# Kernel tuning notes

Measured on AMD Instinct MI355X. Metric: run time of the kernel, lower is better.

The kernel has to match this reference:

```python
import jax, jax.numpy as jnp
import numpy as np

N_NODES = 50000
IN_CH = 128
HIDDEN = 64
HEADS = 2
OUT_CH = 40
N_EDGES = 800000
NEG_SLOPE = 0.2


def gat_layer(x, src, dst, W, att_src, att_dst, bias, concat):
    # x: [N, F_in]; src/dst: [E] (self-loops already appended)
    N = x.shape[0]
    H, C = att_src.shape
    h = (x @ W).reshape(N, H, C)                      # [N, H, C]
    a_s = (h * att_src[None]).sum(-1)                 # [N, H]
    a_d = (h * att_dst[None]).sum(-1)                 # [N, H]
    e = jax.nn.leaky_relu(a_s[src] + a_d[dst], NEG_SLOPE)   # [E, H]
    # numerically-stable segment softmax over incoming edges per dst node
    m = jax.ops.segment_max(e, dst, num_segments=N)   # [N, H]
    m = jnp.where(jnp.isfinite(m), m, 0.0)
    m = jax.lax.stop_gradient(m)
    ex = jnp.exp(e - m[dst])                          # [E, H]
    denom = jax.ops.segment_sum(ex, dst, num_segments=N)    # [N, H]
    alpha = ex / (denom[dst] + 1e-16)                 # [E, H]
    out = jax.ops.segment_sum(alpha[:, :, None] * h[src], dst, num_segments=N)  # [N, H, C]
    out = out.reshape(N, H * C) if concat else out.mean(axis=1)
    return out + bias


def setup_inputs() -> dict:
    key = jax.random.key(0)
    ks = jax.random.split(key, 10)
    node_feat = jax.random.normal(ks[0], (N_NODES, IN_CH), dtype=jnp.float32)
    edge_index = jax.random.randint(ks[1], (2, N_EDGES), 0, N_NODES, dtype=jnp.int64)
    s1 = 1.0 / np.sqrt(IN_CH)
    s2 = 1.0 / np.sqrt(HIDDEN * HEADS)
    return {
        "node_feat": node_feat,
        "edge_index": edge_index,
        "W1": jax.random.normal(ks[2], (IN_CH, HEADS * HIDDEN), dtype=jnp.float32) * s1,
        "att_src1": jax.random.normal(ks[3], (HEADS, HIDDEN), dtype=jnp.float32) * s1,
        "att_dst1": jax.random.normal(ks[4], (HEADS, HIDDEN), dtype=jnp.float32) * s1,
        "b1": jnp.zeros((HEADS * HIDDEN,), dtype=jnp.float32),
        "W2": jax.random.normal(ks[5], (HEADS * HIDDEN, OUT_CH), dtype=jnp.float32) * s2,
        "att_src2": jax.random.normal(ks[6], (1, OUT_CH), dtype=jnp.float32) * s2,
        "att_dst2": jax.random.normal(ks[7], (1, OUT_CH), dtype=jnp.float32) * s2,
        "b2": jnp.zeros((OUT_CH,), dtype=jnp.float32),
    }


def reference(node_feat, edge_index, W1, att_src1, att_dst1, b1, W2, att_src2, att_dst2, b2):
    N = node_feat.shape[0]
    loop = jnp.arange(N, dtype=edge_index.dtype)
    src = jnp.concatenate([edge_index[0], loop])  # add self loops (PyG default)
    dst = jnp.concatenate([edge_index[1], loop])
    # eval mode: dropout is identity; use_bn=False
    x = gat_layer(node_feat, src, dst, W1, att_src1, att_dst1, b1, concat=True)
    x = jax.nn.elu(x)
    x = gat_layer(x, src, dst, W2, att_src2, att_dst2, b2, concat=False)
    return x
```

## Files before the change

### kernel.cpp

```cpp
#include <hip/hip_runtime.h>
#include <hip/hip_bf16.h>

#define N_NODES 50000
#define E0      800000
#define E_TOT   850000

typedef short short8 __attribute__((ext_vector_type(8)));
typedef float floatx4 __attribute__((ext_vector_type(4)));

__device__ __forceinline__ float lrelu(float x) { return x > 0.f ? x : 0.2f * x; }

__device__ __forceinline__ unsigned short f2bf(float f) {
    unsigned int u = __float_as_uint(f);
    u += 0x7fffu + ((u >> 16) & 1u);
    return (unsigned short)(u >> 16);
}
__device__ __forceinline__ float lo_bf(unsigned int p) { return __uint_as_float(p << 16); }
__device__ __forceinline__ float hi_bf(unsigned int p) { return __uint_as_float(p & 0xffff0000u); }

__device__ __forceinline__ short8 pack_bf16x8(float4 a, float4 b) {
    short8 r;
    r[0] = (short)f2bf(a.x); r[1] = (short)f2bf(a.y); r[2] = (short)f2bf(a.z); r[3] = (short)f2bf(a.w);
    r[4] = (short)f2bf(b.x); r[5] = (short)f2bf(b.y); r[6] = (short)f2bf(b.z); r[7] = (short)f2bf(b.w);
    return r;
}

__device__ __forceinline__ void fma8(float2* A, float w, uint4 h) {
    A[0].x += w * lo_bf(h.x); A[0].y += w * hi_bf(h.x);
    A[1].x += w * lo_bf(h.y); A[1].y += w * hi_bf(h.y);
    A[2].x += w * lo_bf(h.z); A[2].y += w * hi_bf(h.z);
    A[3].x += w * lo_bf(h.w); A[3].y += w * hi_bf(h.w);
}

__global__ __launch_bounds__(256) void hist_w(const int* __restrict__ ei, int* __restrict__ ghist,
                                              const float* __restrict__ W1, const float* __restrict__ W2,
                                              unsigned short* __restrict__ Wt1, unsigned short* __restrict__ Wt2) {
    __shared__ int h[256];
    int b = blockIdx.x, t = threadIdx.x;
    h[t] = 0;
    int i = b * 256 + t;
    if (i < 128 * 128) {
        int nn = i >> 7, k = i & 127;
        Wt1[i] = f2bf(W1[k * 128 + nn]);
    } else if (i < 128 * 128 + 48 * 128) {
        int j = i - 128 * 128;
        int nn = j >> 7, k = j & 127;
        Wt2[j] = (nn < 40) ? f2bf(W2[k * 40 + nn]) : (unsigned short)0;
    }
    __syncthreads();
    int base = b * 3328;
    #pragma unroll
    for (int k = 0; k < 13; ++k) {
        int e = base + t + k * 256;
        if (e < E_TOT) {
            int dst = (e < E0) ? ei[E0 + e] : (e - E0);
            atomicAdd(&h[dst >> 8], 1);
        }
    }
    __syncthreads();
    ghist[t * 256 + b] = h[t];
}

__global__ __launch_bounds__(256) void scan_local(const int* __restrict__ src, int* __restrict__ dst,
                                                  int* __restrict__ bsum, int n) {
    __shared__ int wsum[4];
    int t = threadIdx.x, lane = t & 63, wid = t >> 6;
    int idx = blockIdx.x * 1024 + t * 4;
    int4 v = make_int4(0, 0, 0, 0);
    if (idx < n) v = *reinterpret_cast<const int4*>(src + idx);
    int tsum = v.x + v.y + v.z + v.w;
    int sc = tsum;
    #pragma unroll
    for (int s = 1; s < 64; s <<= 1) {
        int up = __shfl_up(sc, s);
        if (lane >= s) sc += up;
    }
    if (lane == 63) wsum[wid] = sc;
    __syncthreads();
    int woff = 0;
    for (int w = 0; w < wid; ++w) woff += wsum[w];
    int b0 = woff + (sc - tsum);
    if (idx < n) {
        int4 o;
        o.x = b0;
        o.y = b0 + v.x;
        o.z = b0 + v.x + v.y;
        o.w = b0 + v.x + v.y + v.z;
        *reinterpret_cast<int4*>(dst + idx) = o;
    }
    if (t == 255) bsum[blockIdx.x] = woff + sc;
}

__global__ __launch_bounds__(256) void scan_addoff(int* __restrict__ arr, const int* __restrict__ bsum,
                                                   int* __restrict__ total, int n, int nb) {
    __shared__ int add_sh;
    int t = threadIdx.x;
    if (t < 64) {
        int v = (t < nb) ? bsum[t] : 0;
        int sc = v;
        #pragma unroll
        for (int s = 1; s < 64; s <<= 1) {
            int up = __shfl_up(sc, s);
            if (t >= s) sc += up;
        }
        if (t == (int)blockIdx.x) add_sh = sc - v;
        if (blockIdx.x == 0 && t == nb - 1) total[0] = sc;
    }
    __syncthreads();
    int idx = blockIdx.x * 1024 + t * 4;
    if (idx < n) {
        int add = add_sh;
        int4 v4 = *reinterpret_cast<int4*>(arr + idx);
        v4.x += add; v4.y += add; v4.z += add; v4.w += add;
        *reinterpret_cast<int4*>(arr + idx) = v4;
    }
}

__global__ __launch_bounds__(256) void scatter1(const int* __restrict__ ei, const int* __restrict__ gbase,
                                                unsigned int* __restrict__ tmpk) {
    __shared__ int cur[256];
    int b = blockIdx.x, t = threadIdx.x;
    cur[t] = gbase[t * 256 + b];
    __syncthreads();
    int base = b * 3328;
    #pragma unroll
    for (int k = 0; k < 13; ++k) {
        int e = base + t + k * 256;
        if (e < E_TOT) {
            int src, dst;
            if (e < E0) { src = ei[e]; dst = ei[E0 + e]; }
            else        { src = dst = e - E0; }
            int pos = atomicAdd(&cur[dst >> 8], 1);
            tmpk[pos] = ((unsigned)dst << 16) | (unsigned)src;
        }
    }
}

__global__ __launch_bounds__(256) void sort_w(const unsigned int* __restrict__ tmpk,
                                              const int* __restrict__ gbase,
                                              const float* __restrict__ a_s, const float* __restrict__ a_d,
                                              unsigned int* __restrict__ keys, uint4* __restrict__ ew,
                                              int* __restrict__ offs) {
    __shared__ unsigned int skey[8192];
    __shared__ unsigned int sorted[8192];
    __shared__ int h2[256], binb[256], cur2[256];
    int q = blockIdx.x, t = threadIdx.x;
    int start = gbase[q * 256];
    int end   = gbase[(q + 1) * 256];
    int n = end - start;
    if (n > 8192) n = 8192;
    h2[t] = 0;
    __syncthreads();
    for (int i = t; i < n; i += 256) {
        unsigned int k = tmpk[start + i];
        skey[i] = k;
        atomicAdd(&h2[(k >> 16) & 255], 1);
    }
    __syncthreads();
    if (t < 64) {
        int carry = 0;
        #pragma unroll
        for (int ch = 0; ch < 4; ++ch) {
            int idx = ch * 64 + t;
            int v = h2[idx];
            int sc = v;
            #pragma unroll
            for (int s = 1; s < 64; s <<= 1) {
                int up = __shfl_up(sc, s);
                if (t >= s) sc += up;
            }
            binb[idx] = sc - v + carry;
            cur2[idx] = sc - v + carry;
            carry += __shfl(sc, 63);
        }
    }
    __syncthreads();
    for (int i = t; i < n; i += 256) {
        unsigned int k = skey[i];
        int pos = atomicAdd(&cur2[(k >> 16) & 255], 1);
        sorted[pos] = k;
    }
    __syncthreads();
    for (int i = t; i < n; i += 256) {
        unsigned int k = sorted[i];
        keys[start + i] = k;
        int src = k & 0xFFFF, dst = k >> 16;
        float2 av = *reinterpret_cast<const float2*>(&a_s[src * 2]);
        float2 dv = *reinterpret_cast<const float2*>(&a_d[dst * 2]);
        uint4 e;
        e.x = k;
        e.y = __float_as_uint(__expf(lrelu(av.x + dv.x)));
        e.z = __float_as_uint(__expf(lrelu(av.y + dv.y)));
        e.w = 0;
        ew[start + i] = e;
    }
    int idx = q * 256 + t;
    if (idx <= N_NODES) offs[idx] = start + binb[t];
}

__global__ __launch_bounds__(256) void gemm1_mfma(const float* __restrict__ X, const unsigned short* __restrict__ Wt,
                                                  const float* __restrict__ asw, const float* __restrict__ adw,
                                                  unsigned short* __restrict__ h1b, float* __restrict__ a_s,
                                                  float* __restrict__ a_d, int nRows) {
    int t = threadIdx.x, lane = t & 63, wave = t >> 6;
    int l15 = lane & 15, g = lane >> 4;
    int r0 = blockIdx.x * 64;
    int row = r0 + wave * 16 + l15;
    bool rv = row < nRows;
    const float* xrow = X + (size_t)(rv ? row : 0) * 128;

    float asv[8], adv[8];
    #pragma unroll
    for (int nt = 0; nt < 8; ++nt) { asv[nt] = asw[nt * 16 + l15]; adv[nt] = adw[nt * 16 + l15]; }

    floatx4 acc[8];
    #pragma unroll
    for (int nt = 0; nt < 8; ++nt) acc[nt] = (floatx4){0.f, 0.f, 0.f, 0.f};

    #pragma unroll
    for (int ks = 0; ks < 4; ++ks) {
        float4 xa = *reinterpret_cast<const float4*>(xrow + ks * 32 + g * 8);
        float4 xb = *reinterpret_cast<const float4*>(xrow + ks * 32 + g * 8 + 4);
        short8 af = pack_bf16x8(xa, xb);
        #pragma unroll
        for (int nt = 0; nt < 8; ++nt) {
            short8 bf = *reinterpret_cast<const short8*>(Wt + (size_t)(nt * 16 + l15) * 128 + ks * 32 + g * 8);
            acc[nt] = __builtin_amdgcn_mfma_f32_16x16x32_bf16(af, bf, acc[nt], 0, 0, 0);
        }
    }

    #pragma unroll
    for (int i = 0; i < 4; ++i) {
        int gr = r0 + wave * 16 + g * 4 + i;
        float s0 = 0.f, d0 = 0.f, s1 = 0.f, d1 = 0.f;
        #pragma unroll
        for (int nt = 0; nt < 4; ++nt) { s0 += acc[nt][i] * asv[nt]; d0 += acc[nt][i] * adv[nt]; }
        #pragma unroll
        for (int nt = 4; nt < 8; ++nt) { s1 += acc[nt][i] * asv[nt]; d1 += acc[nt][i] * adv[nt]; }
        #pragma unroll
        for (int sh = 1; sh < 16; sh <<= 1) {
            s0 += __shfl_xor(s0, sh); d0 += __shfl_xor(d0, sh);
            s1 += __shfl_xor(s1, sh); d1 += __shfl_xor(d1, sh);
        }
        if (gr < nRows) {
            if (l15 == 0) {
                a_s[gr * 2] = s0;     a_d[gr * 2] = d0;
                a_s[gr * 2 + 1] = s1; a_d[gr * 2 + 1] = d1;
            }
            #pragma unroll
            for (int nt = 0; nt < 8; ++nt)
                h1b[(size_t)gr * 128 + nt * 16 + l15] = f2bf(acc[nt][i]);
        }
    }
}

__global__ __launch_bounds__(256) void gemm2_mfma(const unsigned short* __restrict__ X2b,
                                                  const unsigned short* __restrict__ Wt,
                                                  const float* __restrict__ asw, const float* __restrict__ adw,
                                                  unsigned short* __restrict__ h2b, float* __restrict__ a_s,
                                                  float* __restrict__ a_d, int nRows) {
    int t = threadIdx.x, lane = t & 63, wave = t >> 6;
    int l15 = lane & 15, g = lane >> 4;
    int r0 = blockIdx.x * 64;
    int row = r0 + wave * 16 + l15;
    bool rv = row < nRows;
    const unsigned short* xrow = X2b + (size_t)(rv ? row : 0) * 128;

    float asv[3], adv[3];
    #pragma unroll
    for (int nt = 0; nt < 3; ++nt) {
        int col = nt * 16 + l15;
        asv[nt] = (col < 40) ? asw[col] : 0.f;
        adv[nt] = (col < 40) ? adw[col] : 0.f;
    }

    floatx4 acc[3];
    #pragma unroll
    for (int nt = 0; nt < 3; ++nt) acc[nt] = (floatx4){0.f, 0.f, 0.f, 0.f};

    #pragma unroll
    for (int ks = 0; ks < 4; ++ks) {
        short8 af = *reinterpret_cast<const short8*>(xrow + ks * 32 + g * 8);
        #pragma unroll
        for (int nt = 0; nt < 3; ++nt) {
            short8 bf = *reinterpret_cast<const short8*>(Wt + (size_t)(nt * 16 + l15) * 128 + ks * 32 + g * 8);
            acc[nt] = __builtin_amdgcn_mfma_f32_16x16x32_bf16(af, bf, acc[nt], 0, 0, 0);
        }
    }

    #pragma unroll
    for (int i = 0; i < 4; ++i) {
        int gr = r0 + wave * 16 + g * 4 + i;
        float ps = 0.f, pd = 0.f;
        #pragma unroll
        for (int nt = 0; nt < 3; ++nt) { ps += acc[nt][i] * asv[nt]; pd += acc[nt][i] * adv[nt]; }
        #pragma unroll
        for (int sh = 1; sh < 16; sh <<= 1) { ps += __shfl_xor(ps, sh); pd += __shfl_xor(pd, sh); }
        if (gr < nRows) {
            if (l15 == 0) { a_s[gr] = ps; a_d[gr] = pd; }
            #pragma unroll
            for (int nt = 0; nt < 3; ++nt) {
                int col = nt * 16 + l15;
                if (col < 40) h2b[(size_t)gr * 40 + col] = f2bf(acc[nt][i]);
            }
        }
    }
}

__global__ __launch_bounds__(256) void aggregate1(const unsigned short* __restrict__ Hb,
                                                  const uint4* __restrict__ ew, const int* __restrict__ offs,
                                                  const float* __restrict__ bias,
                                                  unsigned short* __restrict__ X2b, int n) {
    int t = threadIdx.x, lane = t & 63, wid = t >> 6;
    int node = blockIdx.x * 4 + wid;
    if (node >= n) return;
    int c = lane & 15, q = lane >> 4, head = c >> 3;
    int beg = offs[node], deg = offs[node + 1] - beg;
    float den = 0.f;
    float2 acc0[4], acc1[4];
    #pragma unroll
    for (int m = 0; m < 4; ++m) { acc0[m] = make_float2(0.f, 0.f); acc1[m] = make_float2(0.f, 0.f); }

    for (int j = 0; j < deg; j += 16) {
        int sE[4]; float wE[4];
        #pragma unroll
        for (int k2 = 0; k2 < 4; ++k2) {
            int idx = j + 4 * k2 + q;
            sE[k2] = 0; wE[k2] = 0.f;
            if (idx < deg) {
                uint4 e = ew[beg + idx];
                sE[k2] = (int)(e.x & 0xFFFF);
                wE[k2] = __uint_as_float(head ? e.z : e.y);
            }
        }
        uint4 h0 = *reinterpret_cast<const uint4*>(&Hb[(size_t)sE[0] * 128 + c * 8]);
        uint4 h1 = *reinterpret_cast<const uint4*>(&Hb[(size_t)sE[1] * 128 + c * 8]);
        uint4 h2 = *reinterpret_cast<const uint4*>(&Hb[(size_t)sE[2] * 128 + c * 8]);
        uint4 h3 = *reinterpret_cast<const uint4*>(&Hb[(size_t)sE[3] * 128 + c * 8]);
        den += wE[0] + wE[1] + wE[2] + wE[3];
        fma8(acc0, wE[0], h0);
        fma8(acc1, wE[1], h1);
        fma8(acc0, wE[2], h2);
        fma8(acc1, wE[3], h3);
    }
    #pragma unroll
    for (int m = 0; m < 4; ++m) { acc0[m].x += acc1[m].x; acc0[m].y += acc1[m].y; }
    den += __shfl_xor(den, 16); den += __shfl_xor(den, 32);
    #pragma unroll
    for (int m = 0; m < 4; ++m) {
        acc0[m].x += __shfl_xor(acc0[m].x, 16); acc0[m].x += __shfl_xor(acc0[m].x, 32);
        acc0[m].y += __shfl_xor(acc0[m].y, 16); acc0[m].y += __shfl_xor(acc0[m].y, 32);
    }
    if (q == 0) {
        float dinv = 1.f / (den + 1e-16f);
        float4 b0 = *reinterpret_cast<const float4*>(&bias[c * 8]);
        float4 b1 = *reinterpret_cast<const float4*>(&bias[c * 8 + 4]);
        float va[8] = {acc0[0].x, acc0[0].y, acc0[1].x, acc0[1].y, acc0[2].x, acc0[2].y, acc0[3].x, acc0[3].y};
        float bb[8] = {b0.x, b0.y, b0.z, b0.w, b1.x, b1.y, b1.z, b1.w};
        float o[8];
        #pragma unroll
        for (int k = 0; k < 8; ++k) {
            float v = va[k] * dinv + bb[k];
            o[k] = v > 0.f ? v : (__expf(v) - 1.f);
        }
        uint4 pk;
        pk.x = (unsigned)f2bf(o[0]) | ((unsigned)f2bf(o[1]) << 16);
        pk.y = (unsigned)f2bf(o[2]) | ((unsigned)f2bf(o[3]) << 16);
        pk.z = (unsigned)f2bf(o[4]) | ((unsigned)f2bf(o[5]) << 16);
        pk.w = (unsigned)f2bf(o[6]) | ((unsigned)f2bf(o[7]) << 16);
        *reinterpret_cast<uint4*>(&X2b[(size_t)node * 128 + c * 8]) = pk;
    }
}

__global__ __launch_bounds__(256) void aggregate2(const unsigned short* __restrict__ Hb,
                                                  const float* __restrict__ a_s, const float* __restrict__ a_d,
                                                  const int* __restrict__ offs, const unsigned int* __restrict__ keys,
                                                  const float* __restrict__ bias, float* __restrict__ out, int n) {
    int t = threadIdx.x, lane = t & 63, wid = t >> 6;
    int node = blockIdx.x * 4 + wid;
    if (node >= n) return;
    int g = lane / 5, c = lane - g * 5;
    bool dead = (g >= 12);
    if (dead) { g = 0; c = 0; }
    int beg = offs[node], deg = offs[node + 1] - beg;
    float adv = a_d[node];
    float den = 0.f;
    float2 acc0[4], acc1[4];
    #pragma unroll
    for (int m = 0; m < 4; ++m) { acc0[m] = make_float2(0.f, 0.f); acc1[m] = make_float2(0.f, 0.f); }

    for (int j = 0; j < deg; j += 24) {
        int j0 = j + g, j1 = j + 12 + g;
        int s0 = 0, s1 = 0;
        float w0 = 0.f, w1v = 0.f;
        if (!dead && j0 < deg) {
            s0 = keys[beg + j0] & 0xFFFF;
            w0 = __expf(lrelu(a_s[s0] + adv));
        }
        if (!dead && j1 < deg) {
            s1 = keys[beg + j1] & 0xFFFF;
            w1v = __expf(lrelu(a_s[s1] + adv));
        }
        uint4 h0 = *reinterpret_cast<const uint4*>(&Hb[(size_t)s0 * 40 + c * 8]);
        uint4 h1 = *reinterpret_cast<const uint4*>(&Hb[(size_t)s1 * 40 + c * 8]);
        den += w0 + w1v;
        fma8(acc0, w0, h0);
        fma8(acc1, w1v, h1);
    }
    #pragma unroll
    for (int m = 0; m < 4; ++m) { acc0[m].x += acc1[m].x; acc0[m].y += acc1[m].y; }
    den += __shfl(den, lane + 30);
    den += __shfl(den, lane + 15);
    {
        float d5 = __shfl(den, lane + 5), d10 = __shfl(den, lane + 10);
        den = den + d5 + d10;
    }
    #pragma unroll
    for (int m = 0; m < 4; ++m) {
        float ax = acc0[m].x, ay = acc0[m].y;
        ax += __shfl(ax, lane + 30); ay += __shfl(ay, lane + 30);
        ax += __shfl(ax, lane + 15); ay += __shfl(ay, lane + 15);
        float ax5 = __shfl(ax, lane + 5),  ay5 = __shfl(ay, lane + 5);
        float ax10 = __shfl(ax, lane + 10), ay10 = __shfl(ay, lane + 10);
        acc0[m].x = ax + ax5 + ax10;
        acc0[m].y = ay + ay5 + ay10;
    }
    if (lane < 5) {
        float dinv = 1.f / (den + 1e-16f);
        float4 b0 = *reinterpret_cast<const float4*>(&bias[c * 8]);
        float4 b1 = *reinterpret_cast<const float4*>(&bias[c * 8 + 4]);
        float4 o0, o1;
        o0.x = acc0[0].x * dinv + b0.x; o0.y = acc0[0].y * dinv + b0.y;
        o0.z = acc0[1].x * dinv + b0.z; o0.w = acc0[1].y * dinv + b0.w;
        o1.x = acc0[2].x * dinv + b1.x; o1.y = acc0[2].y * dinv + b1.y;
        o1.z = acc0[3].x * dinv + b1.z; o1.w = acc0[3].y * dinv + b1.w;
        *reinterpret_cast<float4*>(&out[(size_t)node * 40 + c * 8])     = o0;
        *reinterpret_cast<float4*>(&out[(size_t)node * 40 + c * 8 + 4]) = o1;
    }
}

extern "C" void kernel_launch(void* const* d_in, const int* in_sizes, int n_in,
                              void* d_out, int out_size, void* d_ws, size_t ws_size,
                              hipStream_t stream) {
    (void)in_sizes; (void)n_in; (void)out_size; (void)ws_size;
    const float* x    = (const float*)d_in[0];
    const int*   ei   = (const int*)d_in[1];
    const float* W1   = (const float*)d_in[2];
    const float* as1w = (const float*)d_in[3];
    const float* ad1w = (const float*)d_in[4];
    const float* b1   = (const float*)d_in[5];
    const float* W2   = (const float*)d_in[6];
    const float* as2w = (const float*)d_in[7];
    const float* ad2w = (const float*)d_in[8];
    const float* b2   = (const float*)d_in[9];
    float* out = (float*)d_out;

    float* ws = (float*)d_ws;
    float* h1slot = ws; ws += (size_t)N_NODES * 128;
    float* x2slot = ws; ws += (size_t)N_NODES * 128;
    float* a_s1 = ws; ws += N_NODES * 2;
    float* a_d1 = ws; ws += N_NODES * 2;
    float* a_s2 = ws; ws += N_NODES;
    float* a_d2 = ws; ws += N_NODES;
    float* h2slot = ws; ws += (size_t)N_NODES * 40;
    int* offs  = (int*)ws;
    int* ghist = offs + 50432;
    int* gbase = ghist + 65536;
    int* bsum  = gbase + 65536;
    int* total = bsum + 64;
    unsigned int* tmpk = (unsigned int*)(total + 4);
    unsigned int* keys = tmpk + E_TOT;
    uint4* ew = (uint4*)(keys + E_TOT);
    unsigned short* Wt1 = (unsigned short*)(ew + E_TOT);
    unsigned short* Wt2 = Wt1 + 128 * 128;

    unsigned short* h1b = (unsigned short*)h1slot;
    unsigned short* x2b = (unsigned short*)x2slot;
    unsigned short* h2b = (unsigned short*)h2slot;

    hist_w<<<256, 256, 0, stream>>>(ei, ghist, W1, W2, Wt1, Wt2);
    scan_local<<<64, 256, 0, stream>>>(ghist, gbase, bsum, 65536);
    scan_addoff<<<64, 256, 0, stream>>>(gbase, bsum, total, 65536, 64);
    scatter1<<<256, 256, 0, stream>>>(ei, gbase, tmpk);
    gemm1_mfma<<<(N_NODES + 63) / 64, 256, 0, stream>>>(x, Wt1, as1w, ad1w, h1b, a_s1, a_d1, N_NODES);
    sort_w<<<196, 256, 0, stream>>>(tmpk, gbase, a_s1, a_d1, keys, ew, offs);
    aggregate1<<<(N_NODES + 3) / 4, 256, 0, stream>>>(h1b, ew, offs, b1, x2b, N_NODES);
    gemm2_mfma<<<(N_NODES + 63) / 64, 256, 0, stream>>>(x2b, Wt2, as2w, ad2w, h2b, a_s2, a_d2, N_NODES);
    aggregate2<<<(N_NODES + 3) / 4, 256, 0, stream>>>(h2b, a_s2, a_d2, offs, keys, b2, out, N_NODES);
}
```

Measured before the change: 138.4 us.

## Merge gemm1 with edge scatter and stage edge metadata via wave shuffles

The separate gemm1 and scatter kernels become one launch: the first 782 blocks run the GEMM and the remaining 256 run the edge scatter, so the two independent phases share the device. In both aggregate kernels, each lane loads one edge's source index and weight (coalesced) for up to 64 or 48 edges, then broadcasts them with shuffles instead of reloading them per feature group. The softmax denominator is summed once per edge across the wave. This removes one launch boundary and redundant scattered metadata loads, at the cost of more shuffles and extra lane masking logic.

```diff
diff --git a/kernel.cpp b/kernel.cpp
--- a/kernel.cpp
+++ b/kernel.cpp
@@ -4,6 +4,7 @@
 #define N_NODES 50000
 #define E0      800000
 #define E_TOT   850000
+#define G1_BLOCKS 782
 
 typedef short short8 __attribute__((ext_vector_type(8)));
 typedef float floatx4 __attribute__((ext_vector_type(4)));
@@ -116,22 +117,86 @@
     }
 }
 
-__global__ __launch_bounds__(256) void scatter1(const int* __restrict__ ei, const int* __restrict__ gbase,
-                                                unsigned int* __restrict__ tmpk) {
+__device__ __forceinline__ void gemm1_body(int blk, const float* __restrict__ X, const unsigned short* __restrict__ Wt,
+                                           const float* __restrict__ asw, const float* __restrict__ adw,
+                                           unsigned short* __restrict__ h1b, float* __restrict__ a_s,
+                                           float* __restrict__ a_d, int nRows) {
+    int t = threadIdx.x, lane = t & 63, wave = t >> 6;
+    int l15 = lane & 15, g = lane >> 4;
+    int r0 = blk * 64;
+    int row = r0 + wave * 16 + l15;
+    bool rv = row < nRows;
+    const float* xrow = X + (size_t)(rv ? row : 0) * 128;
+
+    float asv[8], adv[8];
+    #pragma unroll
+    for (int nt = 0; nt < 8; ++nt) { asv[nt] = asw[nt * 16 + l15]; adv[nt] = adw[nt * 16 + l15]; }
+
+    floatx4 acc[8];
+    #pragma unroll
+    for (int nt = 0; nt < 8; ++nt) acc[nt] = (floatx4){0.f, 0.f, 0.f, 0.f};
+
+    #pragma unroll
+    for (int ks = 0; ks < 4; ++ks) {
+        float4 xa = *reinterpret_cast<const float4*>(xrow + ks * 32 + g * 8);
+        float4 xb = *reinterpret_cast<const float4*>(xrow + ks * 32 + g * 8 + 4);
+        short8 af = pack_bf16x8(xa, xb);
+        #pragma unroll
+        for (int nt = 0; nt < 8; ++nt) {
+            short8 bf = *reinterpret_cast<const short8*>(Wt + (size_t)(nt * 16 + l15) * 128 + ks * 32 + g * 8);
+            acc[nt] = __builtin_amdgcn_mfma_f32_16x16x32_bf16(af, bf, acc[nt], 0, 0, 0);
+        }
+    }
+
+    #pragma unroll
+    for (int i = 0; i < 4; ++i) {
+        int gr = r0 + wave * 16 + g * 4 + i;
+        float s0 = 0.f, d0 = 0.f, s1 = 0.f, d1 = 0.f;
+        #pragma unroll
+        for (int nt = 0; nt < 4; ++nt) { s0 += acc[nt][i] * asv[nt]; d0 += acc[nt][i] * adv[nt]; }
+        #pragma unroll
+        for (int nt = 4; nt < 8; ++nt) { s1 += acc[nt][i] * asv[nt]; d1 += acc[nt][i] * adv[nt]; }
+        #pragma unroll
+        for (int sh = 1; sh < 16; sh <<= 1) {
+            s0 += __shfl_xor(s0, sh); d0 += __shfl_xor(d0, sh);
+            s1 += __shfl_xor(s1, sh); d1 += __shfl_xor(d1, sh);
+        }
+        if (gr < nRows) {
+            if (l15 == 0) {
+                a_s[gr * 2] = s0;     a_d[gr * 2] = d0;
+                a_s[gr * 2 + 1] = s1; a_d[gr * 2 + 1] = d1;
+            }
+            #pragma unroll
+            for (int nt = 0; nt < 8; ++nt)
+                h1b[(size_t)gr * 128 + nt * 16 + l15] = f2bf(acc[nt][i]);
+        }
+    }
+}
+
+__global__ __launch_bounds__(256) void gemm1_scatter(const float* __restrict__ X, const unsigned short* __restrict__ Wt,
+                                                     const float* __restrict__ asw, const float* __restrict__ adw,
+                                                     unsigned short* __restrict__ h1b, float* __restrict__ a_s,
+                                                     float* __restrict__ a_d,
+                                                     const int* __restrict__ ei, const int* __restrict__ gbase,
+                                                     unsigned int* __restrict__ tmpk) {
     __shared__ int cur[256];
-    int b = blockIdx.x, t = threadIdx.x;
-    cur[t] = gbase[t * 256 + b];
-    __syncthreads();
-    int base = b * 3328;
-    #pragma unroll
-    for (int k = 0; k < 13; ++k) {
-        int e = base + t + k * 256;
-        if (e < E_TOT) {
-            int src, dst;
-            if (e < E0) { src = ei[e]; dst = ei[E0 + e]; }
-            else        { src = dst = e - E0; }
-            int pos = atomicAdd(&cur[dst >> 8], 1);
-            tmpk[pos] = ((unsigned)dst << 16) | (unsigned)src;
+    if (blockIdx.x < G1_BLOCKS) {
+        gemm1_body(blockIdx.x, X, Wt, asw, adw, h1b, a_s, a_d, N_NODES);
+    } else {
+        int b = blockIdx.x - G1_BLOCKS, t = threadIdx.x;
+        cur[t] = gbase[t * 256 + b];
+        __syncthreads();
+        int base = b * 3328;
+        #pragma unroll
+        for (int k = 0; k < 13; ++k) {
+            int e = base + t + k * 256;
+            if (e < E_TOT) {
+                int src, dst;
+                if (e < E0) { src = ei[e]; dst = ei[E0 + e]; }
+                else        { src = dst = e - E0; }
+                int pos = atomicAdd(&cur[dst >> 8], 1);
+                tmpk[pos] = ((unsigned)dst << 16) | (unsigned)src;
+            }
         }
     }
 }
@@ -198,62 +263,6 @@
     if (idx <= N_NODES) offs[idx] = start + binb[t];
 }
 
-__global__ __launch_bounds__(256) void gemm1_mfma(const float* __restrict__ X, const unsigned short* __restrict__ Wt,
-                                                  const float* __restrict__ asw, const float* __restrict__ adw,
-                                                  unsigned short* __restrict__ h1b, float* __restrict__ a_s,
-                                                  float* __restrict__ a_d, int nRows) {
-    int t = threadIdx.x, lane = t & 63, wave = t >> 6;
-    int l15 = lane & 15, g = lane >> 4;
-    int r0 = blockIdx.x * 64;
-    int row = r0 + wave * 16 + l15;
-    bool rv = row < nRows;
-    const float* xrow = X + (size_t)(rv ? row : 0) * 128;
-
-    float asv[8], adv[8];
-    #pragma unroll
-    for (int nt = 0; nt < 8; ++nt) { asv[nt] = asw[nt * 16 + l15]; adv[nt] = adw[nt * 16 + l15]; }
-
-    floatx4 acc[8];
-    #pragma unroll
-    for (int nt = 0; nt < 8; ++nt) acc[nt] = (floatx4){0.f, 0.f, 0.f, 0.f};
-
-    #pragma unroll
-    for (int ks = 0; ks < 4; ++ks) {
-        float4 xa = *reinterpret_cast<const float4*>(xrow + ks * 32 + g * 8);
-        float4 xb = *reinterpret_cast<const float4*>(xrow + ks * 32 + g * 8 + 4);
-        short8 af = pack_bf16x8(xa, xb);
-        #pragma unroll
-        for (int nt = 0; nt < 8; ++nt) {
-            short8 bf = *reinterpret_cast<const short8*>(Wt + (size_t)(nt * 16 + l15) * 128 + ks * 32 + g * 8);
-            acc[nt] = __builtin_amdgcn_mfma_f32_16x16x32_bf16(af, bf, acc[nt], 0, 0, 0);
-        }
-    }
-
-    #pragma unroll
-    for (int i = 0; i < 4; ++i) {
-        int gr = r0 + wave * 16 + g * 4 + i;
-        float s0 = 0.f, d0 = 0.f, s1 = 0.f, d1 = 0.f;
-        #pragma unroll
-        for (int nt = 0; nt < 4; ++nt) { s0 += acc[nt][i] * asv[nt]; d0 += acc[nt][i] * adv[nt]; }
-        #pragma unroll
-        for (int nt = 4; nt < 8; ++nt) { s1 += acc[nt][i] * asv[nt]; d1 += acc[nt][i] * adv[nt]; }
-        #pragma unroll
-        for (int sh = 1; sh < 16; sh <<= 1) {
-            s0 += __shfl_xor(s0, sh); d0 += __shfl_xor(d0, sh);
-            s1 += __shfl_xor(s1, sh); d1 += __shfl_xor(d1, sh);
-        }
-        if (gr < nRows) {
-            if (l15 == 0) {
-                a_s[gr * 2] = s0;     a_d[gr * 2] = d0;
-                a_s[gr * 2 + 1] = s1; a_d[gr * 2 + 1] = d1;
-            }
-            #pragma unroll
-            for (int nt = 0; nt < 8; ++nt)
-                h1b[(size_t)gr * 128 + nt * 16 + l15] = f2bf(acc[nt][i]);
-        }
-    }
-}
-
 __global__ __launch_bounds__(256) void gemm2_mfma(const unsigned short* __restrict__ X2b,
                                                   const unsigned short* __restrict__ Wt,
                                                   const float* __restrict__ asw, const float* __restrict__ adw,
@@ -316,43 +325,47 @@
     if (node >= n) return;
     int c = lane & 15, q = lane >> 4, head = c >> 3;
     int beg = offs[node], deg = offs[node + 1] - beg;
-    float den = 0.f;
+    float den0 = 0.f, den1 = 0.f;
     float2 acc0[4], acc1[4];
     #pragma unroll
     for (int m = 0; m < 4; ++m) { acc0[m] = make_float2(0.f, 0.f); acc1[m] = make_float2(0.f, 0.f); }
 
-    for (int j = 0; j < deg; j += 16) {
-        int sE[4]; float wE[4];
-        #pragma unroll
-        for (int k2 = 0; k2 < 4; ++k2) {
-            int idx = j + 4 * k2 + q;
-            sE[k2] = 0; wE[k2] = 0.f;
-            if (idx < deg) {
-                uint4 e = ew[beg + idx];
-                sE[k2] = (int)(e.x & 0xFFFF);
-                wE[k2] = __uint_as_float(head ? e.z : e.y);
-            }
-        }
-        uint4 h0 = *reinterpret_cast<const uint4*>(&Hb[(size_t)sE[0] * 128 + c * 8]);
-        uint4 h1 = *reinterpret_cast<const uint4*>(&Hb[(size_t)sE[1] * 128 + c * 8]);
-        uint4 h2 = *reinterpret_cast<const uint4*>(&Hb[(size_t)sE[2] * 128 + c * 8]);
-        uint4 h3 = *reinterpret_cast<const uint4*>(&Hb[(size_t)sE[3] * 128 + c * 8]);
-        den += wE[0] + wE[1] + wE[2] + wE[3];
-        fma8(acc0, wE[0], h0);
-        fma8(acc1, wE[1], h1);
-        fma8(acc0, wE[2], h2);
-        fma8(acc1, wE[3], h3);
+    for (int base = 0; base < deg; base += 64) {
+        int nslots = min(64, deg - base);
+        int s_l = 0; float w0_l = 0.f, w1_l = 0.f;
+        if (lane < nslots) {
+            uint4 e = ew[beg + base + lane];
+            s_l = (int)(e.x & 0xFFFFu);
+            w0_l = __uint_as_float(e.y);
+            w1_l = __uint_as_float(e.z);
+        }
+        den0 += w0_l; den1 += w1_l;
+        for (int j = 0; j < nslots; j += 8) {
+            int j0 = j + q, j1 = j + 4 + q;
+            int   sa  = __shfl(s_l, j0);
+            float wa0 = __shfl(w0_l, j0), wa1 = __shfl(w1_l, j0);
+            int   sb  = __shfl(s_l, j1);
+            float wb0 = __shfl(w0_l, j1), wb1 = __shfl(w1_l, j1);
+            float wa = head ? wa1 : wa0;
+            float wb = head ? wb1 : wb0;
+            uint4 ha = *reinterpret_cast<const uint4*>(&Hb[(size_t)sa * 128 + c * 8]);
+            uint4 hb = *reinterpret_cast<const uint4*>(&Hb[(size_t)sb * 128 + c * 8]);
+            fma8(acc0, wa, ha);
+            fma8(acc1, wb, hb);
+        }
     }
     #pragma unroll
     for (int m = 0; m < 4; ++m) { acc0[m].x += acc1[m].x; acc0[m].y += acc1[m].y; }
-    den += __shfl_xor(den, 16); den += __shfl_xor(den, 32);
+    #pragma unroll
+    for (int sh = 32; sh > 0; sh >>= 1) { den0 += __shfl_xor(den0, sh); den1 += __shfl_xor(den1, sh); }
     #pragma unroll
     for (int m = 0; m < 4; ++m) {
         acc0[m].x += __shfl_xor(acc0[m].x, 16); acc0[m].x += __shfl_xor(acc0[m].x, 32);
         acc0[m].y += __shfl_xor(acc0[m].y, 16); acc0[m].y += __shfl_xor(acc0[m].y, 32);
     }
     if (q == 0) {
-        float dinv = 1.f / (den + 1e-16f);
+        float den = (head ? den1 : den0) + 1e-16f;
+        float dinv = 1.f / den;
         float4 b0 = *reinterpret_cast<const float4*>(&bias[c * 8]);
         float4 b1 = *reinterpret_cast<const float4*>(&bias[c * 8 + 4]);
         float va[8] = {acc0[0].x, acc0[0].y, acc0[1].x, acc0[1].y, acc0[2].x, acc0[2].y, acc0[3].x, acc0[3].y};
@@ -389,32 +402,32 @@
     #pragma unroll
     for (int m = 0; m < 4; ++m) { acc0[m] = make_float2(0.f, 0.f); acc1[m] = make_float2(0.f, 0.f); }
 
-    for (int j = 0; j < deg; j += 24) {
-        int j0 = j + g, j1 = j + 12 + g;
-        int s0 = 0, s1 = 0;
-        float w0 = 0.f, w1v = 0.f;
-        if (!dead && j0 < deg) {
-            s0 = keys[beg + j0] & 0xFFFF;
-            w0 = __expf(lrelu(a_s[s0] + adv));
-        }
-        if (!dead && j1 < deg) {
-            s1 = keys[beg + j1] & 0xFFFF;
-            w1v = __expf(lrelu(a_s[s1] + adv));
-        }
-        uint4 h0 = *reinterpret_cast<const uint4*>(&Hb[(size_t)s0 * 40 + c * 8]);
-        uint4 h1 = *reinterpret_cast<const uint4*>(&Hb[(size_t)s1 * 40 + c * 8]);
-        den += w0 + w1v;
-        fma8(acc0, w0, h0);
-        fma8(acc1, w1v, h1);
+    for (int base = 0; base < deg; base += 48) {
+        int nslots = min(48, deg - base);
+        int s_l = 0; float w_l = 0.f;
+        if (lane < nslots) {
+            s_l = (int)(keys[beg + base + lane] & 0xFFFFu);
+            w_l = __expf(lrelu(a_s[s_l] + adv));
+        }
+        den += w_l;
+        for (int j = 0; j < nslots; j += 24) {
+            int j0 = j + g, j1 = j + 12 + g;
+            int   sa = __shfl(s_l, j0); float wa = __shfl(w_l, j0);
+            int   sb = __shfl(s_l, j1); float wb = __shfl(w_l, j1);
+            uint4 ha = *reinterpret_cast<const uint4*>(&Hb[(size_t)sa * 40 + c * 8]);
+            uint4 hb = *reinterpret_cast<const uint4*>(&Hb[(size_t)sb * 40 + c * 8]);
+            fma8(acc0, wa, ha);
+            fma8(acc1, wb, hb);
+        }
     }
     #pragma unroll
     for (int m = 0; m < 4; ++m) { acc0[m].x += acc1[m].x; acc0[m].y += acc1[m].y; }
-    den += __shfl(den, lane + 30);
-    den += __shfl(den, lane + 15);
-    {
-        float d5 = __shfl(den, lane + 5), d10 = __shfl(den, lane + 10);
-        den = den + d5 + d10;
-    }
+    if (lane >= 60) {
+        #pragma unroll
+        for (int m = 0; m < 4; ++m) acc0[m] = make_float2(0.f, 0.f);
+    }
+    #pragma unroll
+    for (int sh = 32; sh > 0; sh >>= 1) den += __shfl_xor(den, sh);
     #pragma unroll
     for (int m = 0; m < 4; ++m) {
         float ax = acc0[m].x, ay = acc0[m].y;
@@ -481,8 +494,7 @@
     hist_w<<<256, 256, 0, stream>>>(ei, ghist, W1, W2, Wt1, Wt2);
     scan_local<<<64, 256, 0, stream>>>(ghist, gbase, bsum, 65536);
     scan_addoff<<<64, 256, 0, stream>>>(gbase, bsum, total, 65536, 64);
-    scatter1<<<256, 256, 0, stream>>>(ei, gbase, tmpk);
-    gemm1_mfma<<<(N_NODES + 63) / 64, 256, 0, stream>>>(x, Wt1, as1w, ad1w, h1b, a_s1, a_d1, N_NODES);
+    gemm1_scatter<<<G1_BLOCKS + 256, 256, 0, stream>>>(x, Wt1, as1w, ad1w, h1b, a_s1, a_d1, ei, gbase, tmpk);
     sort_w<<<196, 256, 0, stream>>>(tmpk, gbase, a_s1, a_d1, keys, ew, offs);
     aggregate1<<<(N_NODES + 3) / 4, 256, 0, stream>>>(h1b, ew, offs, b1, x2b, N_NODES);
     gemm2_mfma<<<(N_NODES + 63) / 64, 256, 0, stream>>>(x2b, Wt2, as2w, ad2w, h2b, a_s2, a_d2, N_NODES);
```

Result: faster. 124.3 us (median of 3 runs) (-10.2%).
